# Optimization experiments

Measured on AMD Instinct MI355X. Metric: run time of the kernel, lower is better.

## Reference

```python
import jax, jax.numpy as jnp
import numpy as np

B, NY, NX, D = 32, 32, 32, 1024  # batch, patch-grid, hidden


def setup_inputs() -> dict:
    key = jax.random.key(0)
    kx, kl = jax.random.split(key)
    x = jax.random.normal(kx, (B, NY * NX, D), dtype=jnp.float32)
    # per (batch, x-column) valid prefix length along the y patch dim, in [1, NY]
    lengths = jax.random.randint(kl, (B, NX), 1, NY + 1)
    # mask[b, y, x] = 1 if y < lengths[b, x]  (contiguous valid prefix per focused row)
    mask = (jnp.arange(NY)[None, :, None] < lengths[:, None, :]).astype(jnp.int32)
    attention_mask = mask.reshape(B, NY * NX)
    return {"x": x, "attention_mask": attention_mask}


def reference(x, attention_mask):
    b, n, d = x.shape
    # unstack patches: [b, (n_y n_x), d] -> [b, n_y, n_x, d]
    xs = x.reshape(b, NY, NX, d)
    ms = attention_mask.reshape(b, NY, NX)
    # focus_patch_dim(dim=1): roll n_x into batch -> [(b n_x), n_y, d]
    xf = jnp.transpose(xs, (0, 2, 1, 3)).reshape(b * NX, NY, d)
    mf = jnp.transpose(ms, (0, 2, 1)).reshape(b * NX, NY)
    L = mf.sum(axis=1)  # [B'] valid prefix lengths (>=1)
    Lf = L.astype(jnp.float32)
    N = NY
    # PyTorch F.interpolate(mode='linear', align_corners=False) coordinates:
    # src = (t + 0.5) * (L / N) - 0.5, clamped to [0, L-1]
    t = jnp.arange(N, dtype=jnp.float32)
    src = (t[None, :] + 0.5) * (Lf[:, None] / N) - 0.5        # [B', N]
    src = jnp.clip(src, 0.0, Lf[:, None] - 1.0)
    lo = jnp.floor(src).astype(jnp.int32)                     # [B', N]
    hi = jnp.minimum(lo + 1, L[:, None].astype(jnp.int32) - 1)
    w = (src - lo.astype(jnp.float32))[..., None]             # [B', N, 1]
    xlo = jnp.take_along_axis(xf, lo[..., None], axis=1)      # [B', N, d]
    xhi = jnp.take_along_axis(xf, hi[..., None], axis=1)
    out = xlo * (1.0 - w) + xhi * w                           # [B', N, d]
    return out
```

## Files before the change

kernel.cpp:

```cpp
#include <hip/hip_runtime.h>

#define PB 32
#define PNY 32
#define PNX 32
#define PD 1024
#define DCHUNK 256
#define NCHUNK (PD / DCHUNK)

__global__ __launch_bounds__(64) void upip_col_kernel(
    const float* __restrict__ x, const int* __restrict__ mask,
    float* __restrict__ out) {
    const int gb    = blockIdx.x;
    const int chunk = gb & (NCHUNK - 1);
    const int bp    = gb >> 2;
    const int b     = bp >> 5;
    const int xc    = bp & (PNX - 1);

    const int lane = threadIdx.x;
    int mv = 0;
    if (lane < PNY)
        mv = mask[(size_t)b * (PNY * PNX) + (size_t)lane * PNX + xc];
    const int   L  = (int)__popcll(__ballot(mv != 0));
    const float Lf = (float)L;

    const size_t row_stride = (size_t)PNX * PD;
    const float* colp = x + ((size_t)b * (PNY * PNX) + xc) * PD
                          + chunk * DCHUNK + lane * 4;
    float*       outp = out + (size_t)bp * PNY * PD + chunk * DCHUNK + lane * 4;

    const float scale = Lf * 0.03125f;

    int    c0 = -1, c1 = -1;
    float4 r0, r1;

    for (int t = 0; t < PNY; ++t) {
        float src = ((float)t + 0.5f) * scale - 0.5f;
        src = fminf(fmaxf(src, 0.0f), Lf - 1.0f);
        const int   lo = (int)floorf(src);
        const int   hi = min(lo + 1, L - 1);
        const float w  = src - (float)lo;

        if (lo == c1)      { r0 = r1; c0 = c1; }
        else if (lo != c0) { r0 = *reinterpret_cast<const float4*>(
                                 colp + (size_t)lo * row_stride); c0 = lo; }
        if (hi == c0)      { r1 = r0; c1 = c0; }
        else if (hi != c1) { r1 = *reinterpret_cast<const float4*>(
                                 colp + (size_t)hi * row_stride); c1 = hi; }

        const float iw = 1.0f - w;
        float4 o;
        o.x = r0.x * iw + r1.x * w;
        o.y = r0.y * iw + r1.y * w;
        o.z = r0.z * iw + r1.z * w;
        o.w = r0.w * iw + r1.w * w;
        *reinterpret_cast<float4*>(outp + (size_t)t * PD) = o;
    }
}

extern "C" void kernel_launch(void* const* d_in, const int* in_sizes, int n_in,
                              void* d_out, int out_size, void* d_ws, size_t ws_size,
                              hipStream_t stream) {
    const float* x    = (const float*)d_in[0];
    const int*   mask = (const int*)d_in[1];
    float*       out  = (float*)d_out;

    const int nblocks = PB * PNX * NCHUNK;
    upip_col_kernel<<<nblocks, 64, 0, stream>>>(x, mask, out);
}
```

Baseline: 38.52 us.

## Restructure interpolation loop to iterate source rows with prefetched register ring

Reorganizes the per-column interpolation so the outer loop walks valid source rows, keeping a three-deep register ring of rows and issuing the load for row s+3 before emitting the outputs that fall between rows s and s+1. This is meant to hide global load latency that the old loop exposed through data-dependent loads inside the output loop. It adds nested, data-dependent control flow and a few extra registers, and when L is small the edge handling relies on duplicated rows.

```diff
diff --git a/kernel.cpp b/kernel.cpp
--- a/kernel.cpp
+++ b/kernel.cpp
@@ -30,30 +30,37 @@
 
     const float scale = Lf * 0.03125f;
 
-    int    c0 = -1, c1 = -1;
-    float4 r0, r1;
+    float4 ra, rb, rc;
+    ra = *reinterpret_cast<const float4*>(colp);
+    rb = (L > 1) ? *reinterpret_cast<const float4*>(colp + row_stride) : ra;
+    rc = (L > 2) ? *reinterpret_cast<const float4*>(colp + 2 * row_stride) : rb;
 
-    for (int t = 0; t < PNY; ++t) {
-        float src = ((float)t + 0.5f) * scale - 0.5f;
-        src = fminf(fmaxf(src, 0.0f), Lf - 1.0f);
-        const int   lo = (int)floorf(src);
-        const int   hi = min(lo + 1, L - 1);
-        const float w  = src - (float)lo;
+    int t = 0;
+    for (int s = 0; s < L; ++s) {
+        const bool need = (s + 3) <= (L - 1);
+        float4 rd;
+        if (need)
+            rd = *reinterpret_cast<const float4*>(colp + (size_t)(s + 3) * row_stride);
 
-        if (lo == c1)      { r0 = r1; c0 = c1; }
-        else if (lo != c0) { r0 = *reinterpret_cast<const float4*>(
-                                 colp + (size_t)lo * row_stride); c0 = lo; }
-        if (hi == c0)      { r1 = r0; c1 = c0; }
-        else if (hi != c1) { r1 = *reinterpret_cast<const float4*>(
-                                 colp + (size_t)hi * row_stride); c1 = hi; }
+        while (t < PNY) {
+            float src = ((float)t + 0.5f) * scale - 0.5f;
+            src = fminf(fmaxf(src, 0.0f), Lf - 1.0f);
+            const int lo = (int)floorf(src);
+            if (lo != s) break;
+            const float w  = src - (float)lo;
+            const float iw = 1.0f - w;
+            float4 o;
+            o.x = ra.x * iw + rb.x * w;
+            o.y = ra.y * iw + rb.y * w;
+            o.z = ra.z * iw + rb.z * w;
+            o.w = ra.w * iw + rb.w * w;
+            *reinterpret_cast<float4*>(outp + (size_t)t * PD) = o;
+            ++t;
+        }
 
-        const float iw = 1.0f - w;
-        float4 o;
-        o.x = r0.x * iw + r1.x * w;
-        o.y = r0.y * iw + r1.y * w;
-        o.z = r0.z * iw + r1.z * w;
-        o.w = r0.w * iw + r1.w * w;
-        *reinterpret_cast<float4*>(outp + (size_t)t * PD) = o;
+        ra = rb;
+        rb = rc;
+        if (need) rc = rd;
     }
 }
 
```

Measured after the change: 47.38 us. 23.0% more time.
